# Performance work log

Hardware: AMD Instinct MI355X
Metric: run time of the kernel (lower is better)

The kernel has to match this reference:

```python
import jax, jax.numpy as jnp
import numpy as np

TEMPERATURE = 8.0  # sqrt(d_head=64)
MASK_FILL = -1e10


def setup_inputs() -> dict:
    key = jax.random.key(0)
    kq, kk, kv, km = jax.random.split(key, 4)
    B, L, D = 64, 2048, 64
    q = jax.random.normal(kq, (B, L, D), dtype=jnp.float32)
    k = jax.random.normal(kk, (B, L, D), dtype=jnp.float32)
    v = jax.random.normal(kv, (B, L, D), dtype=jnp.float32)
    # boolean mask: True means masked-out position (masked_fill semantics)
    mask = jax.random.bernoulli(km, p=0.3, shape=(B, L, L))
    return {"q": q, "k": k, "v": v, "mask": mask}


def reference(q, k, v, mask):
    # attn scores: [B, Lq, Lk]
    attn = jnp.einsum("bqd,bkd->bqk", q, k) / TEMPERATURE
    attn = jnp.where(mask, MASK_FILL, attn)
    attn = jax.nn.softmax(attn, axis=2)
    # dropout is identity in eval/deterministic reference; explain_weight=None
    output = jnp.einsum("bqk,bkd->bqd", attn, v)
    return (output, attn)
```

## Files before the change

### kernel.cpp

```cpp
#include <hip/hip_runtime.h>

typedef __attribute__((ext_vector_type(8))) short short8;
typedef __attribute__((ext_vector_type(4))) float floatx4;
typedef __attribute__((ext_vector_type(4))) float fx4;
typedef __attribute__((ext_vector_type(4))) unsigned ux4;
typedef __attribute__((ext_vector_type(2))) unsigned ux2;

#define B_DIM 64
#define L_SEQ 2048
#define D_H   64
#define BQ    16
#define QK_SCALE 0.1803368801111137f

#define SC_BYTES  (BQ * L_SEQ * 2)
#define CB_OFF    SC_BYTES
#define RI_OFF    (CB_OFF + 8192)
#define LDS_TOTAL (RI_OFF + 64)

#if defined(__has_builtin)
#  if __has_builtin(__builtin_amdgcn_exp2f)
#    define EXP2(x) __builtin_amdgcn_exp2f(x)
#  else
#    define EXP2(x) exp2f(x)
#  endif
#else
#  define EXP2(x) exp2f(x)
#endif

__device__ __forceinline__ short f2bf(float f) {
    unsigned u = __builtin_bit_cast(unsigned, f);
    u += 0x7FFFu + ((u >> 16) & 1u);
    return (short)(u >> 16);
}
__device__ __forceinline__ float bf2f_lo(unsigned w) {
    return __builtin_bit_cast(float, w << 16);
}
__device__ __forceinline__ float bf2f_hi(unsigned w) {
    return __builtin_bit_cast(float, w & 0xFFFF0000u);
}
__device__ __forceinline__ unsigned pk2bf(float a, float b) {
    unsigned ua = __builtin_bit_cast(unsigned, a);
    unsigned ub = __builtin_bit_cast(unsigned, b);
    ua += 0x7FFFu + ((ua >> 16) & 1u);
    ub += 0x7FFFu + ((ub >> 16) & 1u);
    return (ua >> 16) | (ub & 0xFFFF0000u);
}
__device__ __forceinline__ int sidx(int row, int colbyte) {
    return row * 4096 + (colbyte ^ ((row & 7) << 4));
}

__global__ __launch_bounds__(256) void prep_qk(const float* __restrict__ q,
                                               const float* __restrict__ k,
                                               unsigned short* __restrict__ qb,
                                               unsigned short* __restrict__ kb) {
    size_t i = (size_t)blockIdx.x * 256 + threadIdx.x;
    fx4 q4 = __builtin_nontemporal_load((const fx4*)q + i);
    fx4 k4 = __builtin_nontemporal_load((const fx4*)k + i);
    ux2 qo, ko;
    qo[0] = pk2bf(q4[0] * QK_SCALE, q4[1] * QK_SCALE);
    qo[1] = pk2bf(q4[2] * QK_SCALE, q4[3] * QK_SCALE);
    ko[0] = pk2bf(k4[0], k4[1]);
    ko[1] = pk2bf(k4[2], k4[3]);
    *((ux2*)qb + i) = qo;
    *((ux2*)kb + i) = ko;
}

__global__ __launch_bounds__(256) void prep_vt(const float* __restrict__ v,
                                               unsigned short* __restrict__ vt) {
    __shared__ float tile[64][65];
    const int b  = blockIdx.x >> 5;
    const int kc = (blockIdx.x & 31) * 64;
    const int t  = threadIdx.x;
    {
        const int r = t >> 2, c4 = (t & 3) * 16;
        const float* src = v + ((size_t)b * L_SEQ + kc + r) * D_H + c4;
        #pragma unroll
        for (int j = 0; j < 4; ++j) {
            fx4 f = __builtin_nontemporal_load((const fx4*)(src + j * 4));
            tile[r][c4 + j * 4 + 0] = f[0]; tile[r][c4 + j * 4 + 1] = f[1];
            tile[r][c4 + j * 4 + 2] = f[2]; tile[r][c4 + j * 4 + 3] = f[3];
        }
    }
    __syncthreads();
    const int d = t >> 2, kq = (t & 3) * 16;
    ux4 o0, o1;
    o0[0] = pk2bf(tile[kq + 0][d], tile[kq + 1][d]);
    o0[1] = pk2bf(tile[kq + 2][d], tile[kq + 3][d]);
    o0[2] = pk2bf(tile[kq + 4][d], tile[kq + 5][d]);
    o0[3] = pk2bf(tile[kq + 6][d], tile[kq + 7][d]);
    o1[0] = pk2bf(tile[kq + 8][d], tile[kq + 9][d]);
    o1[1] = pk2bf(tile[kq +10][d], tile[kq +11][d]);
    o1[2] = pk2bf(tile[kq +12][d], tile[kq +13][d]);
    o1[3] = pk2bf(tile[kq +14][d], tile[kq +15][d]);
    unsigned short* dst = vt + ((size_t)b * D_H + d) * L_SEQ + kc + kq;
    *(ux4*)dst = o0;
    *(ux4*)(dst + 8) = o1;
}

template <bool PRE>
__global__ __launch_bounds__(512, 4)
void sdpa_kernel(const float* __restrict__ qf, const float* __restrict__ kf,
                 const float* __restrict__ vf32, const void* __restrict__ mask,
                 const unsigned short* __restrict__ qb,
                 const unsigned short* __restrict__ kb,
                 const unsigned short* __restrict__ vt,
                 float* __restrict__ out, float* __restrict__ attn)
{
    extern __shared__ char lds[];
    float* s_rinv = (float*)(lds + RI_OFF);

    const int tid  = threadIdx.x;
    const int wave = tid >> 6;
    const int lane = tid & 63;
    const int l16  = lane & 15;
    const int l4   = lane >> 4;

    const int bid  = blockIdx.x;
    const int sbid = (bid & 7) * 1024 + (bid >> 3);
    const int b     = sbid >> 7;
    const int qbase = (sbid & 127) * BQ;

    const unsigned* mwords = (const unsigned*)mask;
    bool wordMode = true;
    #pragma unroll 8
    for (int i = 0; i < 64; ++i) {
        unsigned w = mwords[i];
        if (!(w == 0u || w == 1u || w == 0x3F800000u)) wordMode = false;
    }

    const int qa = tid >> 5;
    const int ca = tid & 31;
    const size_t rowbase = ((size_t)b * L_SEQ + qbase + qa) * (size_t)L_SEQ;

    ux2 mm[8];
    if (!wordMode) {
        #pragma unroll
        for (int j = 0; j < 8; ++j)
            mm[j] = __builtin_nontemporal_load(
                (const ux2*)((const unsigned char*)mask + rowbase + ca * 8 + j * 256));
    }

    short8 aq0, aq1;
    if constexpr (PRE) {
        const unsigned short* qrow = qb + ((size_t)b * L_SEQ + qbase + l16) * D_H + l4 * 8;
        aq0 = *(const short8*)(qrow);
        aq1 = *(const short8*)(qrow + 32);
    } else {
        const float* qrow = qf + ((size_t)b * L_SEQ + qbase + l16) * D_H + l4 * 8;
        #pragma unroll
        for (int h = 0; h < 2; ++h) {
            float4 f0 = *(const float4*)(qrow + h * 32);
            float4 f1 = *(const float4*)(qrow + h * 32 + 4);
            short8 a;
            a[0] = f2bf(f0.x * QK_SCALE); a[1] = f2bf(f0.y * QK_SCALE);
            a[2] = f2bf(f0.z * QK_SCALE); a[3] = f2bf(f0.w * QK_SCALE);
            a[4] = f2bf(f1.x * QK_SCALE); a[5] = f2bf(f1.y * QK_SCALE);
            a[6] = f2bf(f1.z * QK_SCALE); a[7] = f2bf(f1.w * QK_SCALE);
            if (h == 0) aq0 = a; else aq1 = a;
        }
    }
    #pragma unroll 2
    for (int t = 0; t < 16; ++t) {
        const int kt = wave * 16 + t;
        floatx4 c = {0.f, 0.f, 0.f, 0.f};
        if constexpr (PRE) {
            const unsigned short* krow = kb + ((size_t)b * L_SEQ + kt * 16 + l16) * D_H + l4 * 8;
            short8 b0 = *(const short8*)(krow);
            short8 b1 = *(const short8*)(krow + 32);
            c = __builtin_amdgcn_mfma_f32_16x16x32_bf16(aq0, b0, c, 0, 0, 0);
            c = __builtin_amdgcn_mfma_f32_16x16x32_bf16(aq1, b1, c, 0, 0, 0);
        } else {
            const float* krow = kf + ((size_t)b * L_SEQ + kt * 16 + l16) * D_H + l4 * 8;
            #pragma unroll
            for (int h = 0; h < 2; ++h) {
                float4 f0 = *(const float4*)(krow + h * 32);
                float4 f1 = *(const float4*)(krow + h * 32 + 4);
                short8 bk;
                bk[0] = f2bf(f0.x); bk[1] = f2bf(f0.y); bk[2] = f2bf(f0.z); bk[3] = f2bf(f0.w);
                bk[4] = f2bf(f1.x); bk[5] = f2bf(f1.y); bk[6] = f2bf(f1.z); bk[7] = f2bf(f1.w);
                c = __builtin_amdgcn_mfma_f32_16x16x32_bf16(h ? aq1 : aq0, bk, c, 0, 0, 0);
            }
        }
        #pragma unroll
        for (int r = 0; r < 4; ++r)
            *(short*)(lds + sidx(l4 * 4 + r, (kt * 16 + l16) * 2)) = f2bf(c[r]);
    }
    __syncthreads();

    ux4 ev[8];
    float psum = 0.f;
    if (!wordMode) {
        #pragma unroll 2
        for (int j = 0; j < 8; ++j) {
            const int col = ca * 8 + j * 256;
            ux4 sw = *(ux4*)(lds + sidx(qa, col * 2));
            float e0 = EXP2(bf2f_lo(sw[0])), e1 = EXP2(bf2f_hi(sw[0]));
            float e2 = EXP2(bf2f_lo(sw[1])), e3 = EXP2(bf2f_hi(sw[1]));
            float e4 = EXP2(bf2f_lo(sw[2])), e5 = EXP2(bf2f_hi(sw[2]));
            float e6 = EXP2(bf2f_lo(sw[3])), e7 = EXP2(bf2f_hi(sw[3]));
            unsigned mx = mm[j][0], my = mm[j][1];
            e0 = (mx & 0x000000FFu) ? 0.f : e0;
            e1 = (mx & 0x0000FF00u) ? 0.f : e1;
            e2 = (mx & 0x00FF0000u) ? 0.f : e2;
            e3 = (mx & 0xFF000000u) ? 0.f : e3;
            e4 = (my & 0x000000FFu) ? 0.f : e4;
            e5 = (my & 0x0000FF00u) ? 0.f : e5;
            e6 = (my & 0x00FF0000u) ? 0.f : e6;
            e7 = (my & 0xFF000000u) ? 0.f : e7;
            psum += ((e0 + e1) + (e2 + e3)) + ((e4 + e5) + (e6 + e7));
            ev[j][0] = pk2bf(e0, e1); ev[j][1] = pk2bf(e2, e3);
            ev[j][2] = pk2bf(e4, e5); ev[j][3] = pk2bf(e6, e7);
            *(ux4*)(lds + sidx(qa, col * 2)) = ev[j];
        }
    } else {
        #pragma unroll 2
        for (int j = 0; j < 8; ++j) {
            const int col = ca * 8 + j * 256;
            ux4 sw = *(ux4*)(lds + sidx(qa, col * 2));
            const unsigned* mp = mwords + rowbase + col;
            ux4 ma = __builtin_nontemporal_load((const ux4*)mp);
            ux4 mb = __builtin_nontemporal_load((const ux4*)mp + 1);
            float e0 = EXP2(bf2f_lo(sw[0])), e1 = EXP2(bf2f_hi(sw[0]));
            float e2 = EXP2(bf2f_lo(sw[1])), e3 = EXP2(bf2f_hi(sw[1]));
            float e4 = EXP2(bf2f_lo(sw[2])), e5 = EXP2(bf2f_hi(sw[2]));
            float e6 = EXP2(bf2f_lo(sw[3])), e7 = EXP2(bf2f_hi(sw[3]));
            e0 = ma[0] ? 0.f : e0; e1 = ma[1] ? 0.f : e1;
            e2 = ma[2] ? 0.f : e2; e3 = ma[3] ? 0.f : e3;
            e4 = mb[0] ? 0.f : e4; e5 = mb[1] ? 0.f : e5;
            e6 = mb[2] ? 0.f : e6; e7 = mb[3] ? 0.f : e7;
            psum += ((e0 + e1) + (e2 + e3)) + ((e4 + e5) + (e6 + e7));
            ev[j][0] = pk2bf(e0, e1); ev[j][1] = pk2bf(e2, e3);
            ev[j][2] = pk2bf(e4, e5); ev[j][3] = pk2bf(e6, e7);
            *(ux4*)(lds + sidx(qa, col * 2)) = ev[j];
        }
    }
    #pragma unroll
    for (int off = 1; off < 32; off <<= 1) psum += __shfl_xor(psum, off, 64);
    const float ri = 1.0f / psum;
    if (ca == 0) s_rinv[qa] = ri;

    {
        float* arow = attn + rowbase;
        #pragma unroll 2
        for (int j = 0; j < 8; ++j) {
            const int col = ca * 8 + j * 256;
            fx4 o0, o1;
            o0[0] = bf2f_lo(ev[j][0]) * ri; o0[1] = bf2f_hi(ev[j][0]) * ri;
            o0[2] = bf2f_lo(ev[j][1]) * ri; o0[3] = bf2f_hi(ev[j][1]) * ri;
            o1[0] = bf2f_lo(ev[j][2]) * ri; o1[1] = bf2f_hi(ev[j][2]) * ri;
            o1[2] = bf2f_lo(ev[j][3]) * ri; o1[3] = bf2f_hi(ev[j][3]) * ri;
            *(fx4*)(arow + col)     = o0;
            *(fx4*)(arow + col + 4) = o1;
        }
    }
    __syncthreads();

    const int dg = wave & 3;
    const int kh = wave >> 2;
    floatx4 oacc = {0.f, 0.f, 0.f, 0.f};

    if constexpr (PRE) {
        const unsigned short* vtb = vt + ((size_t)b * D_H + dg * 16 + l16) * L_SEQ + kh * 32 + l4 * 8;
        short8 vb0 = *(const short8*)(vtb);
        short8 vb1 = *(const short8*)(vtb + 64);
        short8 vb2 = *(const short8*)(vtb + 128);
        short8 vb3 = *(const short8*)(vtb + 192);
        for (int cc = 0; cc < 8; ++cc) {
            short8 vn0, vn1, vn2, vn3;
            if (cc < 7) {
                const unsigned short* vp = vtb + (cc + 1) * 256;
                vn0 = *(const short8*)(vp);
                vn1 = *(const short8*)(vp + 64);
                vn2 = *(const short8*)(vp + 128);
                vn3 = *(const short8*)(vp + 192);
            } else {
                vn0 = vb0; vn1 = vb1; vn2 = vb2; vn3 = vb3;
            }
            const int kbase2 = cc * 512 + kh * 64 + l4 * 16;
            short8 pf0 = *(short8*)(lds + sidx(l16, kbase2));
            oacc = __builtin_amdgcn_mfma_f32_16x16x32_bf16(pf0, vb0, oacc, 0, 0, 0);
            short8 pf1 = *(short8*)(lds + sidx(l16, kbase2 + 128));
            oacc = __builtin_amdgcn_mfma_f32_16x16x32_bf16(pf1, vb1, oacc, 0, 0, 0);
            short8 pf2 = *(short8*)(lds + sidx(l16, kbase2 + 256));
            oacc = __builtin_amdgcn_mfma_f32_16x16x32_bf16(pf2, vb2, oacc, 0, 0, 0);
            short8 pf3 = *(short8*)(lds + sidx(l16, kbase2 + 384));
            oacc = __builtin_amdgcn_mfma_f32_16x16x32_bf16(pf3, vb3, oacc, 0, 0, 0);
            vb0 = vn0; vb1 = vn1; vb2 = vn2; vb3 = vn3;
        }
    } else {
        const float* vp0 = vf32 + ((size_t)b * L_SEQ + kh * 32 + l4 * 8) * D_H + dg * 16 + l16;
        for (int ch = 0; ch < 32; ++ch) {
            const float* vp = vp0 + (size_t)ch * 64 * D_H;
            short8 vfr;
            #pragma unroll
            for (int i = 0; i < 8; ++i) vfr[i] = f2bf(vp[i * D_H]);
            short8 pf = *(short8*)(lds + sidx(l16, ch * 128 + kh * 64 + l4 * 16));
            oacc = __builtin_amdgcn_mfma_f32_16x16x32_bf16(pf, vfr, oacc, 0, 0, 0);
        }
    }

    float* s_comb = (float*)(lds + CB_OFF);
    #pragma unroll
    for (int r = 0; r < 4; ++r)
        s_comb[kh * 1024 + (l4 * 4 + r) * 64 + dg * 16 + l16] = oacc[r];
    __syncthreads();
    if (tid < 256) {
        const int qo = tid >> 4, dc = tid & 15;
        float4 a = *(float4*)(s_comb + qo * 64 + dc * 4);
        float4 c = *(float4*)(s_comb + 1024 + qo * 64 + dc * 4);
        const float rio = s_rinv[qo];
        fx4 o;
        o[0] = (a.x + c.x) * rio; o[1] = (a.y + c.y) * rio;
        o[2] = (a.z + c.z) * rio; o[3] = (a.w + c.w) * rio;
        *(fx4*)(out + ((size_t)b * L_SEQ + qbase + qo) * D_H + dc * 4) = o;
    }
}

extern "C" void kernel_launch(void* const* d_in, const int* in_sizes, int n_in,
                              void* d_out, int out_size, void* d_ws, size_t ws_size,
                              hipStream_t stream) {
    const float* q = (const float*)d_in[0];
    const float* k = (const float*)d_in[1];
    const float* v = (const float*)d_in[2];
    const void* mask = d_in[3];
    float* out  = (float*)d_out;
    float* attn = out + (size_t)B_DIM * L_SEQ * D_H;

    const size_t NE = (size_t)B_DIM * L_SEQ * D_H;
    dim3 grid(B_DIM * (L_SEQ / BQ), 1, 1);
    dim3 block(512, 1, 1);

    if (ws_size >= NE * 2 * 3) {
        unsigned short* qb = (unsigned short*)d_ws;
        unsigned short* kb = qb + NE;
        unsigned short* vt = kb + NE;
        hipLaunchKernelGGL(prep_qk, dim3(8192), dim3(256), 0, stream, q, k, qb, kb);
        hipLaunchKernelGGL(prep_vt, dim3(2048), dim3(256), 0, stream, v, vt);
        hipLaunchKernelGGL((sdpa_kernel<true>), grid, block, LDS_TOTAL, stream,
                           q, k, v, mask, qb, kb, vt, out, attn);
    } else {
        hipLaunchKernelGGL((sdpa_kernel<false>), grid, block, LDS_TOTAL, stream,
                           q, k, v, mask, (const unsigned short*)nullptr,
                           (const unsigned short*)nullptr, (const unsigned short*)nullptr,
                           out, attn);
    }
}
```

Baseline: 812.6 us.

## Restructure main SDPA kernel into chunked double-buffered pipeline with 1024-thread blocks

Replaces the precomputed-path kernel with a new 1024-thread kernel that processes the key dimension in four 512-wide chunks, using a 32 KB double-buffered LDS region instead of a full 64 KB score row buffer. Each chunk runs QK MFMA, a masked exp2 with the mask packed into bits, and a partial PV MFMA, so score, softmax and PV work is interleaved and LDS use per block drops. This is meant to raise occupancy and overlap memory with compute. The cost is more barriers per block and a four-way cross-wave reduction at the end. The fp32 fallback path moves to a separate kernel.

```diff
diff --git a/kernel.cpp b/kernel.cpp
--- a/kernel.cpp
+++ b/kernel.cpp
@@ -10,12 +10,8 @@
 #define L_SEQ 2048
 #define D_H   64
 #define BQ    16
+#define CHUNK 512
 #define QK_SCALE 0.1803368801111137f
-
-#define SC_BYTES  (BQ * L_SEQ * 2)
-#define CB_OFF    SC_BYTES
-#define RI_OFF    (CB_OFF + 8192)
-#define LDS_TOTAL (RI_OFF + 64)
 
 #if defined(__has_builtin)
 #  if __has_builtin(__builtin_amdgcn_exp2f)
@@ -44,6 +40,9 @@
     ua += 0x7FFFu + ((ua >> 16) & 1u);
     ub += 0x7FFFu + ((ub >> 16) & 1u);
     return (ua >> 16) | (ub & 0xFFFF0000u);
+}
+__device__ __forceinline__ int sidxc(int row, int colbyte) {
+    return row * 1024 + (colbyte ^ ((row & 7) << 4));
 }
 __device__ __forceinline__ int sidx(int row, int colbyte) {
     return row * 4096 + (colbyte ^ ((row & 7) << 4));
@@ -97,17 +96,14 @@
     *(ux4*)(dst + 8) = o1;
 }
 
-template <bool PRE>
-__global__ __launch_bounds__(512, 4)
-void sdpa_kernel(const float* __restrict__ qf, const float* __restrict__ kf,
-                 const float* __restrict__ vf32, const void* __restrict__ mask,
-                 const unsigned short* __restrict__ qb,
-                 const unsigned short* __restrict__ kb,
-                 const unsigned short* __restrict__ vt,
-                 float* __restrict__ out, float* __restrict__ attn)
+__global__ __launch_bounds__(1024, 8)
+void sdpa_main(const void* __restrict__ mask,
+               const unsigned short* __restrict__ qb,
+               const unsigned short* __restrict__ kb,
+               const unsigned short* __restrict__ vt,
+               float* __restrict__ out, float* __restrict__ attn)
 {
-    extern __shared__ char lds[];
-    float* s_rinv = (float*)(lds + RI_OFF);
+    __shared__ char lds[32768];
 
     const int tid  = threadIdx.x;
     const int wave = tid >> 6;
@@ -128,6 +124,158 @@
         if (!(w == 0u || w == 1u || w == 0x3F800000u)) wordMode = false;
     }
 
+    const size_t rowbase = ((size_t)b * L_SEQ + qbase + wave) * (size_t)L_SEQ;
+
+    const int dg = wave & 3;
+    const int ks = wave >> 2;
+
+    const unsigned short* qrow = qb + ((size_t)b * L_SEQ + qbase + l16) * D_H + l4 * 8;
+    const unsigned short* kbb  = kb + (size_t)b * L_SEQ * D_H;
+    const unsigned short* vtb  = vt + ((size_t)b * D_H + dg * 16 + l16) * L_SEQ + ks * 128 + l4 * 8;
+
+    ux4 ev[4];
+    float psum = 0.f;
+    floatx4 oacc = {0.f, 0.f, 0.f, 0.f};
+
+    #pragma unroll
+    for (int c = 0; c < 4; ++c) {
+        char* buf = lds + (c & 1) * 16384;
+
+        unsigned mbits;
+        if (!wordMode) {
+            ux2 m = __builtin_nontemporal_load(
+                (const ux2*)((const unsigned char*)mask + rowbase + c * CHUNK + lane * 8));
+            unsigned lo = m[0], hi = m[1];
+            mbits = ((lo & 0x000000FFu) ? 1u : 0u) | ((lo & 0x0000FF00u) ? 2u : 0u) |
+                    ((lo & 0x00FF0000u) ? 4u : 0u) | ((lo & 0xFF000000u) ? 8u : 0u) |
+                    ((hi & 0x000000FFu) ? 16u : 0u) | ((hi & 0x0000FF00u) ? 32u : 0u) |
+                    ((hi & 0x00FF0000u) ? 64u : 0u) | ((hi & 0xFF000000u) ? 128u : 0u);
+        } else {
+            const unsigned* mp = mwords + rowbase + c * CHUNK + lane * 8;
+            ux4 ma = __builtin_nontemporal_load((const ux4*)mp);
+            ux4 mb = __builtin_nontemporal_load((const ux4*)mp + 1);
+            mbits = (ma[0] ? 1u : 0u) | (ma[1] ? 2u : 0u) | (ma[2] ? 4u : 0u) | (ma[3] ? 8u : 0u) |
+                    (mb[0] ? 16u : 0u) | (mb[1] ? 32u : 0u) | (mb[2] ? 64u : 0u) | (mb[3] ? 128u : 0u);
+        }
+
+        {
+            const int kt0 = c * 32 + wave * 2;
+            const unsigned short* kr0 = kbb + (size_t)(kt0 * 16 + l16) * D_H + l4 * 8;
+            const unsigned short* kr1 = kr0 + 16 * D_H;
+            short8 aq0 = *(const short8*)qrow;
+            short8 aq1 = *(const short8*)(qrow + 32);
+            short8 b00 = *(const short8*)kr0;
+            short8 b01 = *(const short8*)(kr0 + 32);
+            short8 b10 = *(const short8*)kr1;
+            short8 b11 = *(const short8*)(kr1 + 32);
+            floatx4 s0 = {0.f, 0.f, 0.f, 0.f};
+            floatx4 s1 = {0.f, 0.f, 0.f, 0.f};
+            s0 = __builtin_amdgcn_mfma_f32_16x16x32_bf16(aq0, b00, s0, 0, 0, 0);
+            s0 = __builtin_amdgcn_mfma_f32_16x16x32_bf16(aq1, b01, s0, 0, 0, 0);
+            s1 = __builtin_amdgcn_mfma_f32_16x16x32_bf16(aq0, b10, s1, 0, 0, 0);
+            s1 = __builtin_amdgcn_mfma_f32_16x16x32_bf16(aq1, b11, s1, 0, 0, 0);
+            const int cb0 = (wave * 2 * 16 + l16) * 2;
+            const int cb1 = cb0 + 32;
+            #pragma unroll
+            for (int r = 0; r < 4; ++r) {
+                *(short*)(buf + sidxc(l4 * 4 + r, cb0)) = f2bf(s0[r]);
+                *(short*)(buf + sidxc(l4 * 4 + r, cb1)) = f2bf(s1[r]);
+            }
+        }
+        __syncthreads();
+
+        {
+            ux4 sw = *(ux4*)(buf + sidxc(wave, lane * 16));
+            float e0 = EXP2(bf2f_lo(sw[0])), e1 = EXP2(bf2f_hi(sw[0]));
+            float e2 = EXP2(bf2f_lo(sw[1])), e3 = EXP2(bf2f_hi(sw[1]));
+            float e4 = EXP2(bf2f_lo(sw[2])), e5 = EXP2(bf2f_hi(sw[2]));
+            float e6 = EXP2(bf2f_lo(sw[3])), e7 = EXP2(bf2f_hi(sw[3]));
+            e0 = (mbits & 1u)   ? 0.f : e0;
+            e1 = (mbits & 2u)   ? 0.f : e1;
+            e2 = (mbits & 4u)   ? 0.f : e2;
+            e3 = (mbits & 8u)   ? 0.f : e3;
+            e4 = (mbits & 16u)  ? 0.f : e4;
+            e5 = (mbits & 32u)  ? 0.f : e5;
+            e6 = (mbits & 64u)  ? 0.f : e6;
+            e7 = (mbits & 128u) ? 0.f : e7;
+            psum += ((e0 + e1) + (e2 + e3)) + ((e4 + e5) + (e6 + e7));
+            ev[c][0] = pk2bf(e0, e1); ev[c][1] = pk2bf(e2, e3);
+            ev[c][2] = pk2bf(e4, e5); ev[c][3] = pk2bf(e6, e7);
+            *(ux4*)(buf + sidxc(wave, lane * 16)) = ev[c];
+        }
+        __syncthreads();
+
+        #pragma unroll
+        for (int s = 0; s < 4; ++s) {
+            short8 vf = *(const short8*)(vtb + c * CHUNK + s * 32);
+            short8 pf = *(short8*)(buf + sidxc(l16, ks * 256 + s * 64 + l4 * 16));
+            oacc = __builtin_amdgcn_mfma_f32_16x16x32_bf16(pf, vf, oacc, 0, 0, 0);
+        }
+    }
+
+    #pragma unroll
+    for (int off = 1; off < 64; off <<= 1) psum += __shfl_xor(psum, off, 64);
+    const float ri = 1.0f / psum;
+
+    {
+        float* arow = attn + rowbase;
+        #pragma unroll
+        for (int c = 0; c < 4; ++c) {
+            fx4 o0, o1;
+            o0[0] = bf2f_lo(ev[c][0]) * ri; o0[1] = bf2f_hi(ev[c][0]) * ri;
+            o0[2] = bf2f_lo(ev[c][1]) * ri; o0[3] = bf2f_hi(ev[c][1]) * ri;
+            o1[0] = bf2f_lo(ev[c][2]) * ri; o1[1] = bf2f_hi(ev[c][2]) * ri;
+            o1[2] = bf2f_lo(ev[c][3]) * ri; o1[3] = bf2f_hi(ev[c][3]) * ri;
+            *(fx4*)(arow + c * CHUNK + lane * 8)     = o0;
+            *(fx4*)(arow + c * CHUNK + lane * 8 + 4) = o1;
+        }
+    }
+
+    float* s_comb = (float*)lds;
+    #pragma unroll
+    for (int r = 0; r < 4; ++r)
+        s_comb[ks * 1024 + (l4 * 4 + r) * 64 + dg * 16 + l16] = oacc[r];
+    __syncthreads();
+    {
+        const int idx = wave * 64 + lane;
+        float o = (s_comb[idx] + s_comb[1024 + idx]) +
+                  (s_comb[2048 + idx] + s_comb[3072 + idx]);
+        out[((size_t)b * L_SEQ + qbase + wave) * D_H + lane] = o * ri;
+    }
+}
+
+#define FB_SC_BYTES  (BQ * L_SEQ * 2)
+#define FB_CB_OFF    FB_SC_BYTES
+#define FB_RI_OFF    (FB_CB_OFF + 8192)
+#define FB_LDS_TOTAL (FB_RI_OFF + 64)
+
+__global__ __launch_bounds__(512, 4)
+void sdpa_fb(const float* __restrict__ qf, const float* __restrict__ kf,
+             const float* __restrict__ vf32, const void* __restrict__ mask,
+             float* __restrict__ out, float* __restrict__ attn)
+{
+    extern __shared__ char lds[];
+    float* s_rinv = (float*)(lds + FB_RI_OFF);
+
+    const int tid  = threadIdx.x;
+    const int wave = tid >> 6;
+    const int lane = tid & 63;
+    const int l16  = lane & 15;
+    const int l4   = lane >> 4;
+
+    const int bid  = blockIdx.x;
+    const int sbid = (bid & 7) * 1024 + (bid >> 3);
+    const int b     = sbid >> 7;
+    const int qbase = (sbid & 127) * BQ;
+
+    const unsigned* mwords = (const unsigned*)mask;
+    bool wordMode = true;
+    #pragma unroll 8
+    for (int i = 0; i < 64; ++i) {
+        unsigned w = mwords[i];
+        if (!(w == 0u || w == 1u || w == 0x3F800000u)) wordMode = false;
+    }
+
     const int qa = tid >> 5;
     const int ca = tid & 31;
     const size_t rowbase = ((size_t)b * L_SEQ + qbase + qa) * (size_t)L_SEQ;
@@ -141,11 +289,7 @@
     }
 
     short8 aq0, aq1;
-    if constexpr (PRE) {
-        const unsigned short* qrow = qb + ((size_t)b * L_SEQ + qbase + l16) * D_H + l4 * 8;
-        aq0 = *(const short8*)(qrow);
-        aq1 = *(const short8*)(qrow + 32);
-    } else {
+    {
         const float* qrow = qf + ((size_t)b * L_SEQ + qbase + l16) * D_H + l4 * 8;
         #pragma unroll
         for (int h = 0; h < 2; ++h) {
@@ -162,24 +306,16 @@
     #pragma unroll 2
     for (int t = 0; t < 16; ++t) {
         const int kt = wave * 16 + t;
+        const float* krow = kf + ((size_t)b * L_SEQ + kt * 16 + l16) * D_H + l4 * 8;
         floatx4 c = {0.f, 0.f, 0.f, 0.f};
-        if constexpr (PRE) {
-            const unsigned short* krow = kb + ((size_t)b * L_SEQ + kt * 16 + l16) * D_H + l4 * 8;
-            short8 b0 = *(const short8*)(krow);
-            short8 b1 = *(const short8*)(krow + 32);
-            c = __builtin_amdgcn_mfma_f32_16x16x32_bf16(aq0, b0, c, 0, 0, 0);
-            c = __builtin_amdgcn_mfma_f32_16x16x32_bf16(aq1, b1, c, 0, 0, 0);
-        } else {
-            const float* krow = kf + ((size_t)b * L_SEQ + kt * 16 + l16) * D_H + l4 * 8;
-            #pragma unroll
-            for (int h = 0; h < 2; ++h) {
-                float4 f0 = *(const float4*)(krow + h * 32);
-                float4 f1 = *(const float4*)(krow + h * 32 + 4);
-                short8 bk;
-                bk[0] = f2bf(f0.x); bk[1] = f2bf(f0.y); bk[2] = f2bf(f0.z); bk[3] = f2bf(f0.w);
-                bk[4] = f2bf(f1.x); bk[5] = f2bf(f1.y); bk[6] = f2bf(f1.z); bk[7] = f2bf(f1.w);
-                c = __builtin_amdgcn_mfma_f32_16x16x32_bf16(h ? aq1 : aq0, bk, c, 0, 0, 0);
-            }
+        #pragma unroll
+        for (int h = 0; h < 2; ++h) {
+            float4 f0 = *(const float4*)(krow + h * 32);
+            float4 f1 = *(const float4*)(krow + h * 32 + 4);
+            short8 bk;
+            bk[0] = f2bf(f0.x); bk[1] = f2bf(f0.y); bk[2] = f2bf(f0.z); bk[3] = f2bf(f0.w);
+            bk[4] = f2bf(f1.x); bk[5] = f2bf(f1.y); bk[6] = f2bf(f1.z); bk[7] = f2bf(f1.w);
+            c = __builtin_amdgcn_mfma_f32_16x16x32_bf16(h ? aq1 : aq0, bk, c, 0, 0, 0);
         }
         #pragma unroll
         for (int r = 0; r < 4; ++r)
@@ -189,50 +325,36 @@
 
     ux4 ev[8];
     float psum = 0.f;
-    if (!wordMode) {
-        #pragma unroll 2
-        for (int j = 0; j < 8; ++j) {
-            const int col = ca * 8 + j * 256;
-            ux4 sw = *(ux4*)(lds + sidx(qa, col * 2));
-            float e0 = EXP2(bf2f_lo(sw[0])), e1 = EXP2(bf2f_hi(sw[0]));
-            float e2 = EXP2(bf2f_lo(sw[1])), e3 = EXP2(bf2f_hi(sw[1]));
-            float e4 = EXP2(bf2f_lo(sw[2])), e5 = EXP2(bf2f_hi(sw[2]));
-            float e6 = EXP2(bf2f_lo(sw[3])), e7 = EXP2(bf2f_hi(sw[3]));
-            unsigned mx = mm[j][0], my = mm[j][1];
-            e0 = (mx & 0x000000FFu) ? 0.f : e0;
-            e1 = (mx & 0x0000FF00u) ? 0.f : e1;
-            e2 = (mx & 0x00FF0000u) ? 0.f : e2;
-            e3 = (mx & 0xFF000000u) ? 0.f : e3;
-            e4 = (my & 0x000000FFu) ? 0.f : e4;
-            e5 = (my & 0x0000FF00u) ? 0.f : e5;
-            e6 = (my & 0x00FF0000u) ? 0.f : e6;
-            e7 = (my & 0xFF000000u) ? 0.f : e7;
-            psum += ((e0 + e1) + (e2 + e3)) + ((e4 + e5) + (e6 + e7));
-            ev[j][0] = pk2bf(e0, e1); ev[j][1] = pk2bf(e2, e3);
-            ev[j][2] = pk2bf(e4, e5); ev[j][3] = pk2bf(e6, e7);
-            *(ux4*)(lds + sidx(qa, col * 2)) = ev[j];
-        }
-    } else {
-        #pragma unroll 2
-        for (int j = 0; j < 8; ++j) {
-            const int col = ca * 8 + j * 256;
-            ux4 sw = *(ux4*)(lds + sidx(qa, col * 2));
+    #pragma unroll 2
+    for (int j = 0; j < 8; ++j) {
+        const int col = ca * 8 + j * 256;
+        ux4 sw = *(ux4*)(lds + sidx(qa, col * 2));
+        unsigned mbits;
+        if (!wordMode) {
+            unsigned lo = mm[j][0], hi = mm[j][1];
+            mbits = ((lo & 0x000000FFu) ? 1u : 0u) | ((lo & 0x0000FF00u) ? 2u : 0u) |
+                    ((lo & 0x00FF0000u) ? 4u : 0u) | ((lo & 0xFF000000u) ? 8u : 0u) |
+                    ((hi & 0x000000FFu) ? 16u : 0u) | ((hi & 0x0000FF00u) ? 32u : 0u) |
+                    ((hi & 0x00FF0000u) ? 64u : 0u) | ((hi & 0xFF000000u) ? 128u : 0u);
+        } else {
             const unsigned* mp = mwords + rowbase + col;
             ux4 ma = __builtin_nontemporal_load((const ux4*)mp);
             ux4 mb = __builtin_nontemporal_load((const ux4*)mp + 1);
-            float e0 = EXP2(bf2f_lo(sw[0])), e1 = EXP2(bf2f_hi(sw[0]));
-            float e2 = EXP2(bf2f_lo(sw[1])), e3 = EXP2(bf2f_hi(sw[1]));
-            float e4 = EXP2(bf2f_lo(sw[2])), e5 = EXP2(bf2f_hi(sw[2]));
-            float e6 = EXP2(bf2f_lo(sw[3])), e7 = EXP2(bf2f_hi(sw[3]));
-            e0 = ma[0] ? 0.f : e0; e1 = ma[1] ? 0.f : e1;
-            e2 = ma[2] ? 0.f : e2; e3 = ma[3] ? 0.f : e3;
-            e4 = mb[0] ? 0.f : e4; e5 = mb[1] ? 0.f : e5;
-            e6 = mb[2] ? 0.f : e6; e7 = mb[3] ? 0.f : e7;
-            psum += ((e0 + e1) + (e2 + e3)) + ((e4 + e5) + (e6 + e7));
-            ev[j][0] = pk2bf(e0, e1); ev[j][1] = pk2bf(e2, e3);
-            ev[j][2] = pk2bf(e4, e5); ev[j][3] = pk2bf(e6, e7);
-            *(ux4*)(lds + sidx(qa, col * 2)) = ev[j];
-        }
+            mbits = (ma[0] ? 1u : 0u) | (ma[1] ? 2u : 0u) | (ma[2] ? 4u : 0u) | (ma[3] ? 8u : 0u) |
+                    (mb[0] ? 16u : 0u) | (mb[1] ? 32u : 0u) | (mb[2] ? 64u : 0u) | (mb[3] ? 128u : 0u);
+        }
+        float e0 = EXP2(bf2f_lo(sw[0])), e1 = EXP2(bf2f_hi(sw[0]));
+        float e2 = EXP2(bf2f_lo(sw[1])), e3 = EXP2(bf2f_hi(sw[1]));
+        float e4 = EXP2(bf2f_lo(sw[2])), e5 = EXP2(bf2f_hi(sw[2]));
+        float e6 = EXP2(bf2f_lo(sw[3])), e7 = EXP2(bf2f_hi(sw[3]));
+        e0 = (mbits & 1u)   ? 0.f : e0;  e1 = (mbits & 2u)   ? 0.f : e1;
+        e2 = (mbits & 4u)   ? 0.f : e2;  e3 = (mbits & 8u)   ? 0.f : e3;
+        e4 = (mbits & 16u)  ? 0.f : e4;  e5 = (mbits & 32u)  ? 0.f : e5;
+        e6 = (mbits & 64u)  ? 0.f : e6;  e7 = (mbits & 128u) ? 0.f : e7;
+        psum += ((e0 + e1) + (e2 + e3)) + ((e4 + e5) + (e6 + e7));
+        ev[j][0] = pk2bf(e0, e1); ev[j][1] = pk2bf(e2, e3);
+        ev[j][2] = pk2bf(e4, e5); ev[j][3] = pk2bf(e6, e7);
+        *(ux4*)(lds + sidx(qa, col * 2)) = ev[j];
     }
     #pragma unroll
     for (int off = 1; off < 32; off <<= 1) psum += __shfl_xor(psum, off, 64);
@@ -258,48 +380,17 @@
     const int dg = wave & 3;
     const int kh = wave >> 2;
     floatx4 oacc = {0.f, 0.f, 0.f, 0.f};
-
-    if constexpr (PRE) {
-        const unsigned short* vtb = vt + ((size_t)b * D_H + dg * 16 + l16) * L_SEQ + kh * 32 + l4 * 8;
-        short8 vb0 = *(const short8*)(vtb);
-        short8 vb1 = *(const short8*)(vtb + 64);
-        short8 vb2 = *(const short8*)(vtb + 128);
-        short8 vb3 = *(const short8*)(vtb + 192);
-        for (int cc = 0; cc < 8; ++cc) {
-            short8 vn0, vn1, vn2, vn3;
-            if (cc < 7) {
-                const unsigned short* vp = vtb + (cc + 1) * 256;
-                vn0 = *(const short8*)(vp);
-                vn1 = *(const short8*)(vp + 64);
-                vn2 = *(const short8*)(vp + 128);
-                vn3 = *(const short8*)(vp + 192);
-            } else {
-                vn0 = vb0; vn1 = vb1; vn2 = vb2; vn3 = vb3;
-            }
-            const int kbase2 = cc * 512 + kh * 64 + l4 * 16;
-            short8 pf0 = *(short8*)(lds + sidx(l16, kbase2));
-            oacc = __builtin_amdgcn_mfma_f32_16x16x32_bf16(pf0, vb0, oacc, 0, 0, 0);
-            short8 pf1 = *(short8*)(lds + sidx(l16, kbase2 + 128));
-            oacc = __builtin_amdgcn_mfma_f32_16x16x32_bf16(pf1, vb1, oacc, 0, 0, 0);
-            short8 pf2 = *(short8*)(lds + sidx(l16, kbase2 + 256));
-            oacc = __builtin_amdgcn_mfma_f32_16x16x32_bf16(pf2, vb2, oacc, 0, 0, 0);
-            short8 pf3 = *(short8*)(lds + sidx(l16, kbase2 + 384));
-            oacc = __builtin_amdgcn_mfma_f32_16x16x32_bf16(pf3, vb3, oacc, 0, 0, 0);
-            vb0 = vn0; vb1 = vn1; vb2 = vn2; vb3 = vn3;
-        }
-    } else {
-        const float* vp0 = vf32 + ((size_t)b * L_SEQ + kh * 32 + l4 * 8) * D_H + dg * 16 + l16;
-        for (int ch = 0; ch < 32; ++ch) {
-            const float* vp = vp0 + (size_t)ch * 64 * D_H;
-            short8 vfr;
-            #pragma unroll
-            for (int i = 0; i < 8; ++i) vfr[i] = f2bf(vp[i * D_H]);
-            short8 pf = *(short8*)(lds + sidx(l16, ch * 128 + kh * 64 + l4 * 16));
-            oacc = __builtin_amdgcn_mfma_f32_16x16x32_bf16(pf, vfr, oacc, 0, 0, 0);
-        }
-    }
-
-    float* s_comb = (float*)(lds + CB_OFF);
+    const float* vp0 = vf32 + ((size_t)b * L_SEQ + kh * 32 + l4 * 8) * D_H + dg * 16 + l16;
+    for (int ch = 0; ch < 32; ++ch) {
+        const float* vp = vp0 + (size_t)ch * 64 * D_H;
+        short8 vfr;
+        #pragma unroll
+        for (int i = 0; i < 8; ++i) vfr[i] = f2bf(vp[i * D_H]);
+        short8 pf = *(short8*)(lds + sidx(l16, ch * 128 + kh * 64 + l4 * 16));
+        oacc = __builtin_amdgcn_mfma_f32_16x16x32_bf16(pf, vfr, oacc, 0, 0, 0);
+    }
+
+    float* s_comb = (float*)(lds + FB_CB_OFF);
     #pragma unroll
     for (int r = 0; r < 4; ++r)
         s_comb[kh * 1024 + (l4 * 4 + r) * 64 + dg * 16 + l16] = oacc[r];
@@ -328,7 +419,6 @@
 
     const size_t NE = (size_t)B_DIM * L_SEQ * D_H;
     dim3 grid(B_DIM * (L_SEQ / BQ), 1, 1);
-    dim3 block(512, 1, 1);
 
     if (ws_size >= NE * 2 * 3) {
         unsigned short* qb = (unsigned short*)d_ws;
@@ -336,12 +426,10 @@
         unsigned short* vt = kb + NE;
         hipLaunchKernelGGL(prep_qk, dim3(8192), dim3(256), 0, stream, q, k, qb, kb);
         hipLaunchKernelGGL(prep_vt, dim3(2048), dim3(256), 0, stream, v, vt);
-        hipLaunchKernelGGL((sdpa_kernel<true>), grid, block, LDS_TOTAL, stream,
-                           q, k, v, mask, qb, kb, vt, out, attn);
+        hipLaunchKernelGGL(sdpa_main, grid, dim3(1024, 1, 1), 0, stream,
+                           mask, qb, kb, vt, out, attn);
     } else {
-        hipLaunchKernelGGL((sdpa_kernel<false>), grid, block, LDS_TOTAL, stream,
-                           q, k, v, mask, (const unsigned short*)nullptr,
-                           (const unsigned short*)nullptr, (const unsigned short*)nullptr,
-                           out, attn);
-    }
-}
+        hipLaunchKernelGGL(sdpa_fb, grid, dim3(512, 1, 1), FB_LDS_TOTAL, stream,
+                           q, k, v, mask, out, attn);
+    }
+}
```

Result: slower. 1.608 ms (+97.9%).
